# Optimization experiments

Measured on AMD Instinct MI355X. Metric: run time of the kernel, lower is better.

Reference implementation:

```python
import jax, jax.numpy as jnp
import numpy as np

HIDDEN = 4096
N_HEADS = 32
HEAD_DIM = HIDDEN // N_HEADS  # 128
ROPE_BASE = 10000.0
NEG_INF = -1e9  # stands in for torch.finfo(dtype).min in the additive mask


def rotate_half(x):
    x1 = x[..., : x.shape[-1] // 2]
    x2 = x[..., x.shape[-1] // 2 :]
    return jnp.concatenate((-x2, x1), axis=-1)


def rope_tables(seq_len, dtype=jnp.float32):
    # RotaryEmbedding: inv_freq = 1/base^(arange(0,dim,2)/dim); emb = cat(freqs, freqs)
    inv_freq = 1.0 / (ROPE_BASE ** (jnp.arange(0, HEAD_DIM, 2, dtype=jnp.float32) / HEAD_DIM))
    t = jnp.arange(seq_len, dtype=jnp.float32)
    freqs = jnp.einsum('s,d->sd', t, inv_freq)          # [S, HEAD_DIM/2]
    emb = jnp.concatenate((freqs, freqs), axis=-1)      # [S, HEAD_DIM]
    return jnp.cos(emb).astype(dtype), jnp.sin(emb).astype(dtype)


def setup_inputs() -> dict:
    key = jax.random.key(0)
    k0, k1, k2 = jax.random.split(key, 3)
    B, S = 1, 2048
    hidden_states = jax.random.normal(k0, (B, S, HIDDEN), dtype=jnp.float32)
    W_pack = jax.random.normal(k1, (3 * HIDDEN, HIDDEN), dtype=jnp.float32) * 0.02
    W_o = jax.random.normal(k2, (HIDDEN, HIDDEN), dtype=jnp.float32) * 0.02
    position_ids = jnp.broadcast_to(jnp.arange(S, dtype=jnp.int32)[None, :], (B, S))
    # additive causal mask [B, 1, S, S]
    causal = jnp.tril(jnp.ones((S, S), dtype=bool))
    attention_mask = jnp.where(causal, 0.0, NEG_INF).astype(jnp.float32)[None, None, :, :]
    attention_mask = jnp.broadcast_to(attention_mask, (B, 1, S, S))
    return {
        'hidden_states': hidden_states,
        'attention_mask': attention_mask,
        'position_ids': position_ids,
        'W_pack': W_pack,
        'W_o': W_o,
    }


def reference(hidden_states, attention_mask, position_ids, W_pack, W_o):
    B, S, H = hidden_states.shape
    norm_factor = 1.0 / np.sqrt(HEAD_DIM)

    # fused QKV projection: Linear(H, 3H, bias=False)
    proj = jnp.einsum('bsh,ph->bsp', hidden_states, W_pack)        # [B, S, 3H]
    q, k, v = jnp.split(proj, 3, axis=-1)

    def to_heads(x):
        return x.reshape(B, S, N_HEADS, HEAD_DIM).transpose(0, 2, 1, 3)  # [B, nH, S, D]

    q, k, v = to_heads(q), to_heads(k), to_heads(v)

    # RoPE (gather per position_ids, matching apply_rotary_pos_emb with unsqueeze_dim=1)
    cos_t, sin_t = rope_tables(S, hidden_states.dtype)
    cos = cos_t[position_ids][:, None, :, :]  # [B, 1, S, D]
    sin = sin_t[position_ids][:, None, :, :]
    q = q * cos + rotate_half(q) * sin
    k = k * cos + rotate_half(k) * sin

    # manual QK^T / softmax / AV (prefill: KV-cache update is a plain copy of cur)
    scores = jnp.einsum('bhqd,bhkd->bhqk', q, k) * norm_factor + attention_mask
    probs = jax.nn.softmax(scores, axis=-1)
    attn = jnp.einsum('bhqk,bhkd->bhqd', probs, v)                 # [B, nH, S, D]

    attn = attn.transpose(0, 2, 1, 3).reshape(B, S, H)
    return jnp.einsum('bsh,oh->bso', attn, W_o)
```

## Files before the change

kernel.cpp:

```cpp
#include <hip/hip_runtime.h>
#include <math.h>

typedef __bf16 bf16x8 __attribute__((ext_vector_type(8)));
typedef __bf16 bf16x4 __attribute__((ext_vector_type(4)));
typedef float f32x4 __attribute__((ext_vector_type(4)));

#define S_LEN 2048
#define NHEADS 32
#define DHEAD 128
#define HID 4096

__device__ __forceinline__ void gld16(const void* g, void* l) {
  __builtin_amdgcn_global_load_lds(
      (const __attribute__((address_space(1))) unsigned int*)g,
      (__attribute__((address_space(3))) unsigned int*)l, 16, 0, 0);
}

__global__ __launch_bounds__(256) void cvt_k(const float4* __restrict__ in,
                                             __bf16* __restrict__ out, int n4) {
  int i = blockIdx.x * 256 + threadIdx.x;
  if (i >= n4) return;
  float4 f = in[i];
  bf16x4 o;
  o[0] = (__bf16)f.x; o[1] = (__bf16)f.y; o[2] = (__bf16)f.z; o[3] = (__bf16)f.w;
  *(bf16x4*)(out + (size_t)i * 4) = o;
}

template <int ND, int KD, int EPI>
__global__ __launch_bounds__(256) void gemm_bt(const __bf16* __restrict__ A,
                                               const __bf16* __restrict__ B,
                                               float* __restrict__ C,
                                               __bf16* __restrict__ Qh,
                                               __bf16* __restrict__ Kh,
                                               __bf16* __restrict__ Vh) {
  const int bn = blockIdx.x, bm = blockIdx.y;
  const int t = threadIdx.x;
  const int w = t >> 6, l = t & 63, quad = l >> 4, l15 = l & 15;
  const int wr = w >> 1, wc = w & 1;

  __shared__ __align__(16) __bf16 As[128 * 32];
  __shared__ __align__(16) __bf16 Bs[128 * 32];

  const f32x4 zero4 = {0.f, 0.f, 0.f, 0.f};
  f32x4 acc[4][4];
#pragma unroll
  for (int i = 0; i < 4; ++i)
#pragma unroll
    for (int j = 0; j < 4; ++j) acc[i][j] = zero4;

  const __bf16* Ab = A + (size_t)bm * 128 * KD;
  const __bf16* Bb = B + (size_t)bn * 128 * KD;

  for (int k0 = 0; k0 < KD; k0 += 32) {
    __syncthreads();
#pragma unroll
    for (int j = 0; j < 2; ++j) {
      const int c = j * 256 + t;
      const int row = c >> 2, kcs = c & 3;
      const int kc = (kcs - (row >> 1)) & 3;
      const int cb = j * 256 + w * 64;
      gld16(Ab + (size_t)row * KD + k0 + kc * 8, As + (size_t)cb * 8);
      gld16(Bb + (size_t)row * KD + k0 + kc * 8, Bs + (size_t)cb * 8);
    }
    __syncthreads();
    bf16x8 af[4], bf_[4];
    const int cq = (quad + (l15 >> 1)) & 3;
#pragma unroll
    for (int mi = 0; mi < 4; ++mi)
      af[mi] = *(const bf16x8*)(As + (wr * 64 + mi * 16 + l15) * 32 + cq * 8);
#pragma unroll
    for (int ni = 0; ni < 4; ++ni)
      bf_[ni] = *(const bf16x8*)(Bs + (wc * 64 + ni * 16 + l15) * 32 + cq * 8);
#pragma unroll
    for (int mi = 0; mi < 4; ++mi)
#pragma unroll
      for (int ni = 0; ni < 4; ++ni)
        acc[mi][ni] = __builtin_amdgcn_mfma_f32_16x16x32_bf16(af[mi], bf_[ni], acc[mi][ni], 0, 0, 0);
  }

#pragma unroll
  for (int mi = 0; mi < 4; ++mi)
#pragma unroll
    for (int ni = 0; ni < 4; ++ni)
#pragma unroll
      for (int r = 0; r < 4; ++r) {
        const int row = bm * 128 + wr * 64 + mi * 16 + quad * 4 + r;
        const int col = bn * 128 + wc * 64 + ni * 16 + l15;
        const float v = acc[mi][ni][r];
        if constexpr (EPI == 0) {
          C[(size_t)row * ND + col] = v;
        } else {
          const int part = col >> 12;
          const int cl = col & 4095;
          const int hh = cl >> 7, d = cl & 127;
          __bf16* dst = (part == 0) ? Qh : (part == 1) ? Kh : Vh;
          dst[(size_t)(hh * S_LEN + row) * DHEAD + d] = (__bf16)v;
        }
      }
}

__global__ __launch_bounds__(256) void rope_k(__bf16* __restrict__ Q, __bf16* __restrict__ K) {
  const int idx = blockIdx.x * 256 + threadIdx.x;
  const int i = idx & 63;
  const int s = (idx >> 6) & (S_LEN - 1);
  const int h = idx >> 17;
  const float inv_freq = __expf(-9.210340371976184f * (float)i * (1.0f / 64.0f));
  float sn, cs;
  sincosf((float)s * inv_freq, &sn, &cs);
  const float nf = 0.08838834764831845f;
  const size_t base = (size_t)(h * S_LEN + s) * DHEAD;
  const float q0 = (float)Q[base + i], q1 = (float)Q[base + i + 64];
  Q[base + i]      = (__bf16)((q0 * cs - q1 * sn) * nf);
  Q[base + i + 64] = (__bf16)((q1 * cs + q0 * sn) * nf);
  const float k0 = (float)K[base + i], k1 = (float)K[base + i + 64];
  K[base + i]      = (__bf16)(k0 * cs - k1 * sn);
  K[base + i + 64] = (__bf16)(k1 * cs + k0 * sn);
}

__global__ __launch_bounds__(256) void vtrans_k(const __bf16* __restrict__ Vh,
                                                __bf16* __restrict__ Vt) {
  __shared__ __align__(16) __bf16 tile[64][72];
  const int s0 = blockIdx.x * 64, d0 = blockIdx.y * 64, h = blockIdx.z;
  const int t = threadIdx.x;
#pragma unroll
  for (int j = 0; j < 2; ++j) {
    const int idx = j * 256 + t;
    const int r = idx >> 3, c8 = idx & 7;
    const bf16x8 v = *(const bf16x8*)(Vh + (size_t)(h * S_LEN + s0 + r) * DHEAD + d0 + c8 * 8);
    *(bf16x8*)(&tile[r][c8 * 8]) = v;
  }
  __syncthreads();
#pragma unroll
  for (int j = 0; j < 2; ++j) {
    const int idx = j * 256 + t;
    const int rd = idx >> 3, c8 = idx & 7;
    bf16x8 v;
#pragma unroll
    for (int i = 0; i < 8; ++i) v[i] = tile[c8 * 8 + i][rd];
    *(bf16x8*)(Vt + (size_t)(h * DHEAD + d0 + rd) * S_LEN + s0 + c8 * 8) = v;
  }
}

__global__ __launch_bounds__(256) void flash_k(const __bf16* __restrict__ Qh,
                                               const __bf16* __restrict__ Kh,
                                               const __bf16* __restrict__ Vt,
                                               __bf16* __restrict__ ctx) {
  const int qt = (int)gridDim.x - 1 - (int)blockIdx.x;
  const int h = blockIdx.y;
  const int t = threadIdx.x;
  const int w = t >> 6, l = t & 63, quad = l >> 4, l15 = l & 15;

  __shared__ __align__(16) __bf16 Ks[64 * 128];
  __shared__ __align__(16) __bf16 Vts[128 * 64];
  __shared__ __align__(16) __bf16 Ps[4][32 * 76];

  const int q0 = qt * 128;
  const int qbase = q0 + w * 32;

  bf16x8 qf[2][4];
#pragma unroll
  for (int mi = 0; mi < 2; ++mi)
#pragma unroll
    for (int ks = 0; ks < 4; ++ks)
      qf[mi][ks] = *(const bf16x8*)(Qh + (size_t)(h * S_LEN + qbase + mi * 16 + l15) * DHEAD +
                                    ks * 32 + quad * 8);

  const f32x4 zero4 = {0.f, 0.f, 0.f, 0.f};
  f32x4 o[2][8];
  float rs[2][4];
#pragma unroll
  for (int mi = 0; mi < 2; ++mi) {
#pragma unroll
    for (int ni = 0; ni < 8; ++ni) o[mi][ni] = zero4;
#pragma unroll
    for (int r = 0; r < 4; ++r) rs[mi][r] = 0.f;
  }

  const int nkt = 2 * (qt + 1);
  for (int kt = 0; kt < nkt; ++kt) {
    const int k0 = kt * 64;
    __syncthreads();
#pragma unroll
    for (int j = 0; j < 4; ++j) {
      const int c = j * 256 + t;
      const int row = c >> 4, dcs = c & 15;
      const int dc = (dcs - row) & 15;
      gld16(Kh + (size_t)(h * S_LEN + k0 + row) * DHEAD + dc * 8,
            Ks + (size_t)(j * 256 + w * 64) * 8);
    }
#pragma unroll
    for (int j = 0; j < 4; ++j) {
      const int c = j * 256 + t;
      const int d = c >> 3, kcs = c & 7;
      const int kc = (kcs - d) & 7;
      gld16(Vt + (size_t)(h * DHEAD + d) * S_LEN + k0 + kc * 8,
            Vts + (size_t)(j * 256 + w * 64) * 8);
    }
    __syncthreads();

    if (k0 <= qbase + 31) {
      f32x4 sacc[2][4];
#pragma unroll
      for (int mi = 0; mi < 2; ++mi)
#pragma unroll
        for (int ni = 0; ni < 4; ++ni) sacc[mi][ni] = zero4;
#pragma unroll
      for (int ks = 0; ks < 4; ++ks) {
        bf16x8 bk[4];
#pragma unroll
        for (int ni = 0; ni < 4; ++ni)
          bk[ni] = *(const bf16x8*)(Ks + (ni * 16 + l15) * 128 +
                                    ((ks * 4 + quad + l15) & 15) * 8);
#pragma unroll
        for (int mi = 0; mi < 2; ++mi)
#pragma unroll
          for (int ni = 0; ni < 4; ++ni)
            sacc[mi][ni] = __builtin_amdgcn_mfma_f32_16x16x32_bf16(qf[mi][ks], bk[ni],
                                                                   sacc[mi][ni], 0, 0, 0);
      }

      const bool need_mask = (k0 + 63 > qbase);
      if (need_mask) {
#pragma unroll
        for (int mi = 0; mi < 2; ++mi)
#pragma unroll
          for (int ni = 0; ni < 4; ++ni)
#pragma unroll
            for (int r = 0; r < 4; ++r) {
              float p = __expf(sacc[mi][ni][r]);
              if (k0 + ni * 16 + l15 > qbase + mi * 16 + quad * 4 + r) p = 0.f;
              rs[mi][r] += p;
              Ps[w][(mi * 16 + quad * 4 + r) * 76 + ni * 16 + l15] = (__bf16)p;
            }
      } else {
#pragma unroll
        for (int mi = 0; mi < 2; ++mi)
#pragma unroll
          for (int ni = 0; ni < 4; ++ni)
#pragma unroll
            for (int r = 0; r < 4; ++r) {
              const float p = __expf(sacc[mi][ni][r]);
              rs[mi][r] += p;
              Ps[w][(mi * 16 + quad * 4 + r) * 76 + ni * 16 + l15] = (__bf16)p;
            }
      }

#pragma unroll
      for (int ks = 0; ks < 2; ++ks) {
        bf16x8 ap[2];
#pragma unroll
        for (int mi = 0; mi < 2; ++mi)
          ap[mi] = *(const bf16x8*)(&Ps[w][(mi * 16 + l15) * 76 + ks * 32 + quad * 8]);
#pragma unroll
        for (int ni = 0; ni < 8; ++ni) {
          const bf16x8 bv = *(const bf16x8*)(Vts + (ni * 16 + l15) * 64 +
                                             ((ks * 4 + quad + l15) & 7) * 8);
#pragma unroll
          for (int mi = 0; mi < 2; ++mi)
            o[mi][ni] = __builtin_amdgcn_mfma_f32_16x16x32_bf16(ap[mi], bv, o[mi][ni], 0, 0, 0);
        }
      }
    }
  }

#pragma unroll
  for (int mi = 0; mi < 2; ++mi)
#pragma unroll
    for (int r = 0; r < 4; ++r) {
      float s = rs[mi][r];
#pragma unroll
      for (int off = 1; off < 16; off <<= 1) s += __shfl_xor(s, off);
      const float inv = 1.f / s;
      const size_t row = (size_t)qbase + mi * 16 + quad * 4 + r;
#pragma unroll
      for (int ni = 0; ni < 8; ++ni)
        ctx[row * HID + h * DHEAD + ni * 16 + l15] = (__bf16)(o[mi][ni][r] * inv);
    }
}

extern "C" void kernel_launch(void* const* d_in, const int* in_sizes, int n_in,
                              void* d_out, int out_size, void* d_ws, size_t ws_size,
                              hipStream_t stream) {
  const float* hs = (const float*)d_in[0];
  const float* Wp = (const float*)d_in[3];
  const float* Wo = (const float*)d_in[4];
  float* out = (float*)d_out;

  char* p = (char*)d_ws;
  auto carve = [&](size_t elems) {
    __bf16* r = (__bf16*)p;
    p += ((elems * sizeof(__bf16) + 255) / 256) * 256;
    return r;
  };
  __bf16* Xb  = carve((size_t)S_LEN * HID);
  __bf16* Wpb = carve((size_t)3 * HID * HID);
  __bf16* Wob = carve((size_t)HID * HID);
  __bf16* Qh  = carve((size_t)S_LEN * HID);
  __bf16* Kh  = carve((size_t)S_LEN * HID);
  __bf16* Vh  = carve((size_t)S_LEN * HID);
  __bf16* Vt  = carve((size_t)S_LEN * HID);
  __bf16* ctx = carve((size_t)S_LEN * HID);

  cvt_k<<<(S_LEN * HID / 4) / 256, 256, 0, stream>>>((const float4*)hs, Xb, S_LEN * HID / 4);
  cvt_k<<<(3 * HID * HID / 4) / 256, 256, 0, stream>>>((const float4*)Wp, Wpb, 3 * HID * HID / 4);
  cvt_k<<<(HID * HID / 4) / 256, 256, 0, stream>>>((const float4*)Wo, Wob, HID * HID / 4);

  gemm_bt<3 * HID, HID, 1><<<dim3(96, 16), 256, 0, stream>>>(Xb, Wpb, nullptr, Qh, Kh, Vh);
  rope_k<<<(NHEADS * S_LEN * 64) / 256, 256, 0, stream>>>(Qh, Kh);
  vtrans_k<<<dim3(S_LEN / 64, DHEAD / 64, NHEADS), 256, 0, stream>>>(Vh, Vt);
  flash_k<<<dim3(S_LEN / 128, NHEADS), 256, 0, stream>>>(Qh, Kh, Vt, ctx);
  gemm_bt<HID, HID, 0><<<dim3(32, 16), 256, 0, stream>>>(ctx, Wob, out, nullptr, nullptr, nullptr);
}
```

Measured before the change: 853.6 us.

## Fuse fp32-to-bf16 conversion into GEMM loads with register prefetch

Removes the three separate conversion kernels and makes both GEMMs read fp32 operands directly, converting to bf16 in registers before storing into shared memory. The global loads for the next k-tile are issued into registers ahead of the MFMA work, replacing the asynchronous global_load_lds path. The flash kernel now writes its context in fp32 so the output projection can consume it with the same kernel, and RoPE uses the fast sincos intrinsic. This avoids separate conversion passes and their extra memory traffic, but each GEMM block now reads twice the bytes per tile, reconverts weights in every block that touches them, and needs more registers and VALU work.

Measured after the change: 905.5 us. 6.1% more time.

```diff
diff --git a/kernel.cpp b/kernel.cpp
--- a/kernel.cpp
+++ b/kernel.cpp
@@ -2,7 +2,6 @@
 #include <math.h>
 
 typedef __bf16 bf16x8 __attribute__((ext_vector_type(8)));
-typedef __bf16 bf16x4 __attribute__((ext_vector_type(4)));
 typedef float f32x4 __attribute__((ext_vector_type(4)));
 
 #define S_LEN 2048
@@ -16,23 +15,13 @@
       (__attribute__((address_space(3))) unsigned int*)l, 16, 0, 0);
 }
 
-__global__ __launch_bounds__(256) void cvt_k(const float4* __restrict__ in,
-                                             __bf16* __restrict__ out, int n4) {
-  int i = blockIdx.x * 256 + threadIdx.x;
-  if (i >= n4) return;
-  float4 f = in[i];
-  bf16x4 o;
-  o[0] = (__bf16)f.x; o[1] = (__bf16)f.y; o[2] = (__bf16)f.z; o[3] = (__bf16)f.w;
-  *(bf16x4*)(out + (size_t)i * 4) = o;
-}
-
 template <int ND, int KD, int EPI>
-__global__ __launch_bounds__(256) void gemm_bt(const __bf16* __restrict__ A,
-                                               const __bf16* __restrict__ B,
-                                               float* __restrict__ C,
-                                               __bf16* __restrict__ Qh,
-                                               __bf16* __restrict__ Kh,
-                                               __bf16* __restrict__ Vh) {
+__global__ __launch_bounds__(256) void gemm_f32bt(const float* __restrict__ A,
+                                                  const float* __restrict__ B,
+                                                  float* __restrict__ C,
+                                                  __bf16* __restrict__ Qh,
+                                                  __bf16* __restrict__ Kh,
+                                                  __bf16* __restrict__ Vh) {
   const int bn = blockIdx.x, bm = blockIdx.y;
   const int t = threadIdx.x;
   const int w = t >> 6, l = t & 63, quad = l >> 4, l15 = l & 15;
@@ -48,34 +37,61 @@
 #pragma unroll
     for (int j = 0; j < 4; ++j) acc[i][j] = zero4;
 
-  const __bf16* Ab = A + (size_t)bm * 128 * KD;
-  const __bf16* Bb = B + (size_t)bn * 128 * KD;
-
+  const float* Ab = A + (size_t)bm * 128 * KD;
+  const float* Bb = B + (size_t)bn * 128 * KD;
+
+  const int row0 = t >> 2, kc0 = t & 3;
+  const int slot = (kc0 + (row0 >> 1)) & 3;
+
+  float4 pa[2][2], pb[2][2];
+  auto issue = [&](int k0) {
+    const float* a0 = Ab + (size_t)row0 * KD + k0 + kc0 * 8;
+    const float* a1 = a0 + (size_t)64 * KD;
+    pa[0][0] = *(const float4*)a0; pa[0][1] = *(const float4*)(a0 + 4);
+    pa[1][0] = *(const float4*)a1; pa[1][1] = *(const float4*)(a1 + 4);
+    const float* b0 = Bb + (size_t)row0 * KD + k0 + kc0 * 8;
+    const float* b1 = b0 + (size_t)64 * KD;
+    pb[0][0] = *(const float4*)b0; pb[0][1] = *(const float4*)(b0 + 4);
+    pb[1][0] = *(const float4*)b1; pb[1][1] = *(const float4*)(b1 + 4);
+  };
+  auto stage = [&]() {
+#pragma unroll
+    for (int j = 0; j < 2; ++j) {
+      const int row = row0 + j * 64;
+      bf16x8 va, vb;
+      va[0] = (__bf16)pa[j][0].x; va[1] = (__bf16)pa[j][0].y;
+      va[2] = (__bf16)pa[j][0].z; va[3] = (__bf16)pa[j][0].w;
+      va[4] = (__bf16)pa[j][1].x; va[5] = (__bf16)pa[j][1].y;
+      va[6] = (__bf16)pa[j][1].z; va[7] = (__bf16)pa[j][1].w;
+      vb[0] = (__bf16)pb[j][0].x; vb[1] = (__bf16)pb[j][0].y;
+      vb[2] = (__bf16)pb[j][0].z; vb[3] = (__bf16)pb[j][0].w;
+      vb[4] = (__bf16)pb[j][1].x; vb[5] = (__bf16)pb[j][1].y;
+      vb[6] = (__bf16)pb[j][1].z; vb[7] = (__bf16)pb[j][1].w;
+      *(bf16x8*)(As + ((row << 2) + slot) * 8) = va;
+      *(bf16x8*)(Bs + ((row << 2) + slot) * 8) = vb;
+    }
+  };
+
+  issue(0);
   for (int k0 = 0; k0 < KD; k0 += 32) {
     __syncthreads();
-#pragma unroll
-    for (int j = 0; j < 2; ++j) {
-      const int c = j * 256 + t;
-      const int row = c >> 2, kcs = c & 3;
-      const int kc = (kcs - (row >> 1)) & 3;
-      const int cb = j * 256 + w * 64;
-      gld16(Ab + (size_t)row * KD + k0 + kc * 8, As + (size_t)cb * 8);
-      gld16(Bb + (size_t)row * KD + k0 + kc * 8, Bs + (size_t)cb * 8);
-    }
+    stage();
     __syncthreads();
-    bf16x8 af[4], bf_[4];
+    if (k0 + 32 < KD) issue(k0 + 32);
+
+    bf16x8 af[4], bfr[4];
     const int cq = (quad + (l15 >> 1)) & 3;
 #pragma unroll
     for (int mi = 0; mi < 4; ++mi)
       af[mi] = *(const bf16x8*)(As + (wr * 64 + mi * 16 + l15) * 32 + cq * 8);
 #pragma unroll
     for (int ni = 0; ni < 4; ++ni)
-      bf_[ni] = *(const bf16x8*)(Bs + (wc * 64 + ni * 16 + l15) * 32 + cq * 8);
+      bfr[ni] = *(const bf16x8*)(Bs + (wc * 64 + ni * 16 + l15) * 32 + cq * 8);
 #pragma unroll
     for (int mi = 0; mi < 4; ++mi)
 #pragma unroll
       for (int ni = 0; ni < 4; ++ni)
-        acc[mi][ni] = __builtin_amdgcn_mfma_f32_16x16x32_bf16(af[mi], bf_[ni], acc[mi][ni], 0, 0, 0);
+        acc[mi][ni] = __builtin_amdgcn_mfma_f32_16x16x32_bf16(af[mi], bfr[ni], acc[mi][ni], 0, 0, 0);
   }
 
 #pragma unroll
@@ -106,7 +122,7 @@
   const int h = idx >> 17;
   const float inv_freq = __expf(-9.210340371976184f * (float)i * (1.0f / 64.0f));
   float sn, cs;
-  sincosf((float)s * inv_freq, &sn, &cs);
+  __sincosf((float)s * inv_freq, &sn, &cs);
   const float nf = 0.08838834764831845f;
   const size_t base = (size_t)(h * S_LEN + s) * DHEAD;
   const float q0 = (float)Q[base + i], q1 = (float)Q[base + i + 64];
@@ -144,7 +160,7 @@
 __global__ __launch_bounds__(256) void flash_k(const __bf16* __restrict__ Qh,
                                                const __bf16* __restrict__ Kh,
                                                const __bf16* __restrict__ Vt,
-                                               __bf16* __restrict__ ctx) {
+                                               float* __restrict__ ctx) {
   const int qt = (int)gridDim.x - 1 - (int)blockIdx.x;
   const int h = blockIdx.y;
   const int t = threadIdx.x;
@@ -274,7 +290,7 @@
       const size_t row = (size_t)qbase + mi * 16 + quad * 4 + r;
 #pragma unroll
       for (int ni = 0; ni < 8; ++ni)
-        ctx[row * HID + h * DHEAD + ni * 16 + l15] = (__bf16)(o[mi][ni][r] * inv);
+        ctx[row * HID + h * DHEAD + ni * 16 + l15] = o[mi][ni][r] * inv;
     }
 }
 
@@ -287,27 +303,20 @@
   float* out = (float*)d_out;
 
   char* p = (char*)d_ws;
-  auto carve = [&](size_t elems) {
+  auto carveb = [&](size_t elems) {
     __bf16* r = (__bf16*)p;
     p += ((elems * sizeof(__bf16) + 255) / 256) * 256;
     return r;
   };
-  __bf16* Xb  = carve((size_t)S_LEN * HID);
-  __bf16* Wpb = carve((size_t)3 * HID * HID);
-  __bf16* Wob = carve((size_t)HID * HID);
-  __bf16* Qh  = carve((size_t)S_LEN * HID);
-  __bf16* Kh  = carve((size_t)S_LEN * HID);
-  __bf16* Vh  = carve((size_t)S_LEN * HID);
-  __bf16* Vt  = carve((size_t)S_LEN * HID);
-  __bf16* ctx = carve((size_t)S_LEN * HID);
-
-  cvt_k<<<(S_LEN * HID / 4) / 256, 256, 0, stream>>>((const float4*)hs, Xb, S_LEN * HID / 4);
-  cvt_k<<<(3 * HID * HID / 4) / 256, 256, 0, stream>>>((const float4*)Wp, Wpb, 3 * HID * HID / 4);
-  cvt_k<<<(HID * HID / 4) / 256, 256, 0, stream>>>((const float4*)Wo, Wob, HID * HID / 4);
-
-  gemm_bt<3 * HID, HID, 1><<<dim3(96, 16), 256, 0, stream>>>(Xb, Wpb, nullptr, Qh, Kh, Vh);
+  __bf16* Qh  = carveb((size_t)S_LEN * HID);
+  __bf16* Kh  = carveb((size_t)S_LEN * HID);
+  __bf16* Vh  = carveb((size_t)S_LEN * HID);
+  __bf16* Vt  = carveb((size_t)S_LEN * HID);
+  float*  ctx = (float*)p;
+
+  gemm_f32bt<3 * HID, HID, 1><<<dim3(96, 16), 256, 0, stream>>>(hs, Wp, nullptr, Qh, Kh, Vh);
   rope_k<<<(NHEADS * S_LEN * 64) / 256, 256, 0, stream>>>(Qh, Kh);
   vtrans_k<<<dim3(S_LEN / 64, DHEAD / 64, NHEADS), 256, 0, stream>>>(Vh, Vt);
   flash_k<<<dim3(S_LEN / 128, NHEADS), 256, 0, stream>>>(Qh, Kh, Vt, ctx);
-  gemm_bt<HID, HID, 0><<<dim3(32, 16), 256, 0, stream>>>(ctx, Wob, out, nullptr, nullptr, nullptr);
-}
+  gemm_f32bt<HID, HID, 0><<<dim3(32, 16), 256, 0, stream>>>(ctx, Wo, out, nullptr, nullptr, nullptr);
+}
```
